# Optimization experiments

Measured on AMD Instinct MI355X. Metric: run time of the kernel, lower is better.

The kernel has to match this reference:

```python
import jax, jax.numpy as jnp
import numpy as np

B, L, D, H = 4, 2048, 1024, 16
d = D // H  # head_dim = 64
EPS = 1e-5
ROPE_BASE = 10000.0


def _rope_tables(seq_len, dim):
    inv_freq = 1.0 / (ROPE_BASE ** (jnp.arange(0, dim, 2, dtype=jnp.float32) / dim))
    t = jnp.arange(seq_len, dtype=jnp.float32)
    freqs = jnp.outer(t, inv_freq)                  # (L, d/2)
    emb = jnp.concatenate([freqs, freqs], axis=-1)  # (L, d)
    return jnp.cos(emb), jnp.sin(emb)


def _rotate_half(x):
    x1, x2 = jnp.split(x, 2, axis=-1)
    return jnp.concatenate([-x2, x1], axis=-1)


def setup_inputs() -> dict:
    key = jax.random.key(0)
    ks = jax.random.split(key, 5)
    x = jax.random.normal(ks[0], (B, L, D), dtype=jnp.float32)
    attn_mask = jnp.ones((B, 1, L, L), dtype=jnp.float32)
    conversion_mask = jax.random.uniform(ks[1], (B, L), dtype=jnp.float32)
    Wqkuv = jax.random.normal(ks[2], (D, 4 * D), dtype=jnp.float32) * (1.0 / np.sqrt(D))
    Wout = jax.random.normal(ks[3], (D, D), dtype=jnp.float32) * (1.0 / np.sqrt(D))
    ln_gamma = jnp.ones((d,), dtype=jnp.float32)
    ln_beta = jnp.zeros((d,), dtype=jnp.float32)
    conv_bias = jax.random.normal(ks[4], (H,), dtype=jnp.float32) * 0.02
    return {"x": x, "attn_mask": attn_mask, "conversion_mask": conversion_mask,
            "Wqkuv": Wqkuv, "Wout": Wout, "ln_gamma": ln_gamma,
            "ln_beta": ln_beta, "conv_bias": conv_bias}


def reference(x, attn_mask, conversion_mask, Wqkuv, Wout, ln_gamma, ln_beta, conv_bias):
    # qkuv projection with SiLU
    qkuv = jax.nn.silu(jnp.einsum('bld,de->ble', x, Wqkuv))  # (B, L, 4D)
    q, k, v, u = jnp.split(qkuv, 4, axis=-1)
    # reshape to (B, H, L, d)
    to_heads = lambda t: t.reshape(B, L, H, d).transpose(0, 2, 1, 3)
    q, k, v, u = map(to_heads, (q, k, v, u))
    # RoPE
    cos, sin = _rope_tables(L, d)            # (L, d)
    cos = cos[None, None]                    # (1,1,L,d)
    sin = sin[None, None]
    q = q * cos + _rotate_half(q) * sin
    k = k * cos + _rotate_half(k) * sin
    # scores + conversion bias + SiLU + multiplicative mask
    scores = jnp.einsum('bhld,bhmd->bhlm', q, k) / jnp.sqrt(jnp.float32(d))
    scores = scores + conversion_mask[:, None, None, :] * conv_bias[None, :, None, None]
    scores = jax.nn.silu(scores)
    scores = scores * attn_mask
    # attend, LayerNorm over head_dim, SiLU-gate with u
    attn_out = jnp.einsum('bhlm,bhmd->bhld', scores, v)
    mu = jnp.mean(attn_out, axis=-1, keepdims=True)
    var = jnp.var(attn_out, axis=-1, keepdims=True)
    attn_out = (attn_out - mu) / jnp.sqrt(var + EPS) * ln_gamma + ln_beta
    attn_out = attn_out * u
    attn_out = attn_out.transpose(0, 2, 1, 3).reshape(B, L, D)
    return jnp.einsum('bld,de->ble', attn_out, Wout)
```

## Files before the change

kernel.cpp:

```cpp
#include <hip/hip_runtime.h>
#include <math.h>

#define B_ 4
#define L_ 2048
#define D_ 1024
#define H_ 16

typedef __attribute__((ext_vector_type(4))) float f32x4;
typedef __attribute__((ext_vector_type(2))) float f32x2;
typedef __attribute__((ext_vector_type(8))) short s16x8;
typedef __attribute__((ext_vector_type(4))) short s16x4;
typedef __attribute__((ext_vector_type(4))) unsigned short u16x4;

__device__ __forceinline__ unsigned short f2bf(float f) {
  unsigned int u = __float_as_uint(f);
  u += 0x7fffu + ((u >> 16) & 1u);
  return (unsigned short)(u >> 16);
}
__device__ __forceinline__ float b2f(unsigned short s) {
  return __uint_as_float(((unsigned int)s) << 16);
}

__device__ __forceinline__ f32x4 mfma16x16x16_bf16(s16x4 a, s16x4 b, f32x4 c) {
#if __has_builtin(__builtin_amdgcn_mfma_f32_16x16x16bf16_1k)
  return __builtin_amdgcn_mfma_f32_16x16x16bf16_1k(a, b, c, 0, 0, 0);
#else
  f32x4 d;
  asm volatile("v_mfma_f32_16x16x16_bf16 %0, %1, %2, %3"
               : "=v"(d)
               : "v"(a), "v"(b), "v"(c));
  return d;
#endif
}

__global__ __launch_bounds__(256) void conv_x(const float* __restrict__ x,
                                              unsigned short* __restrict__ xb, int n4) {
  int i = blockIdx.x * 256 + threadIdx.x;
  if (i < n4) {
    f32x4 v = *(const f32x4*)(x + (size_t)i * 4);
    u16x4 o;
#pragma unroll
    for (int j = 0; j < 4; ++j) o[j] = f2bf(v[j]);
    *(u16x4*)(xb + (size_t)i * 4) = o;
  }
}

__global__ __launch_bounds__(256) void trans_w(const float* __restrict__ W,
                                               unsigned short* __restrict__ Wt,
                                               int K, int N) {
  __shared__ float T[64][65];
  const int k0 = blockIdx.y * 64, n0 = blockIdx.x * 64;
  const int tid = threadIdx.x;
#pragma unroll
  for (int i = 0; i < 16; ++i) {
    int e = tid + i * 256;
    int r = e >> 6, c = e & 63;
    T[r][c] = W[(size_t)(k0 + r) * N + n0 + c];
  }
  __syncthreads();
#pragma unroll
  for (int i = 0; i < 16; ++i) {
    int e = tid + i * 256;
    int r = e >> 6, c = e & 63;
    Wt[(size_t)(n0 + r) * K + k0 + c] = f2bf(T[c][r]);
  }
}

__global__ __launch_bounds__(256) void rope_tab(f32x2* __restrict__ tab) {
  int i = blockIdx.x * 256 + threadIdx.x;
  int l = i >> 5, j = i & 31;
  float inv = expf(-(float)j * (9.210340371976184f / 32.0f));
  float ang = (float)l * inv;
  f32x2 cs;
  cs[0] = cosf(ang);
  cs[1] = sinf(ang);
  tab[i] = cs;
}

template <int MODE>
__global__ __launch_bounds__(256) void gemm_bf16(const unsigned short* __restrict__ A,
                                                 const unsigned short* __restrict__ Bt,
                                                 void* __restrict__ Cp,
                                                 int M, int N, int K) {
  alignas(16) __shared__ unsigned short As[128][40];
  alignas(16) __shared__ unsigned short Bs[128][40];
  const int tid = threadIdx.x;
  const int lane = tid & 63, w = tid >> 6;
  const int quad = lane >> 4, l15 = lane & 15;
  const int wr = w >> 1, wc = w & 1;
  const int m0 = blockIdx.y * 128, n0 = blockIdx.x * 128;
  f32x4 acc[4][4] = {};
  for (int k0 = 0; k0 < K; k0 += 32) {
#pragma unroll
    for (int i = 0; i < 2; ++i) {
      int ch = tid + i * 256;
      int r = ch >> 2, c = ch & 3;
      *(s16x8*)&As[r][c * 8] = *(const s16x8*)(A + (size_t)(m0 + r) * K + k0 + c * 8);
      *(s16x8*)&Bs[r][c * 8] = *(const s16x8*)(Bt + (size_t)(n0 + r) * K + k0 + c * 8);
    }
    __syncthreads();
    s16x8 af[4], bf[4];
#pragma unroll
    for (int mi = 0; mi < 4; ++mi) af[mi] = *(const s16x8*)&As[wr * 64 + mi * 16 + l15][quad * 8];
#pragma unroll
    for (int nj = 0; nj < 4; ++nj) bf[nj] = *(const s16x8*)&Bs[wc * 64 + nj * 16 + l15][quad * 8];
#pragma unroll
    for (int mi = 0; mi < 4; ++mi)
#pragma unroll
      for (int nj = 0; nj < 4; ++nj)
        acc[mi][nj] = __builtin_amdgcn_mfma_f32_16x16x32_bf16(af[mi], bf[nj], acc[mi][nj], 0, 0, 0);
    __syncthreads();
  }
#pragma unroll
  for (int mi = 0; mi < 4; ++mi)
#pragma unroll
    for (int nj = 0; nj < 4; ++nj)
#pragma unroll
      for (int reg = 0; reg < 4; ++reg) {
        int rg = m0 + wr * 64 + mi * 16 + quad * 4 + reg;
        int cg = n0 + wc * 64 + nj * 16 + l15;
        float v = acc[mi][nj][reg];
        if (MODE == 1) {
          v = v / (1.0f + __expf(-v));
          ((unsigned short*)Cp)[(size_t)rg * N + cg] = f2bf(v);
        } else {
          ((float*)Cp)[(size_t)rg * N + cg] = v;
        }
      }
}

__global__ __launch_bounds__(256) void rope_conv(unsigned short* __restrict__ qk,
                                                 unsigned short* __restrict__ vt,
                                                 const f32x2* __restrict__ tab) {
  alignas(16) __shared__ unsigned short Vsh[64][72];
  const int tid = threadIdx.x;
  const int bh = blockIdx.y, b = bh >> 4, h = bh & 15;
  const int l0 = blockIdx.x * 64;
#pragma unroll
  for (int i = 0; i < 2; ++i) {
    int p = tid + i * 256;
    int row = p >> 3, c4 = p & 7;
    int l = l0 + row;
    size_t base = (size_t)(b * L_ + l) * 4096 + h * 64 + c4 * 4;
#pragma unroll
    for (int t = 0; t < 2; ++t) {
      size_t o = base + (size_t)t * 1024;
      u16x4 lo = *(u16x4*)(qk + o);
      u16x4 hi = *(u16x4*)(qk + o + 32);
      u16x4 nlo, nhi;
#pragma unroll
      for (int jj = 0; jj < 4; ++jj) {
        f32x2 cs = tab[l * 32 + c4 * 4 + jj];
        float fl = b2f(lo[jj]), fh = b2f(hi[jj]);
        nlo[jj] = f2bf(fl * cs[0] - fh * cs[1]);
        nhi[jj] = f2bf(fh * cs[0] + fl * cs[1]);
      }
      *(u16x4*)(qk + o) = nlo;
      *(u16x4*)(qk + o + 32) = nhi;
    }
  }
#pragma unroll
  for (int i = 0; i < 2; ++i) {
    int ch = tid + i * 256;
    int row = ch >> 3, c8 = ch & 7;
    *(s16x8*)&Vsh[row][c8 * 8] =
        *(const s16x8*)(qk + (size_t)(b * L_ + l0 + row) * 4096 + 2048 + h * 64 + c8 * 8);
  }
  __syncthreads();
#pragma unroll
  for (int i = 0; i < 2; ++i) {
    int ch = tid + i * 256;
    int drow = ch >> 3, c8 = ch & 7;
    s16x8 o;
#pragma unroll
    for (int jj = 0; jj < 8; ++jj) o[jj] = (short)Vsh[c8 * 8 + jj][drow];
    *(s16x8*)(vt + (size_t)(bh * 64 + drow) * 2048 + l0 + c8 * 8) = o;
  }
}

__global__ __launch_bounds__(256) void attn_mfma(
    const unsigned short* __restrict__ qk, const unsigned short* __restrict__ vt,
    const float* __restrict__ amask, const float* __restrict__ cmask,
    const float* __restrict__ cbias, const float* __restrict__ gamma,
    const float* __restrict__ beta, unsigned short* __restrict__ attng) {
  alignas(16) __shared__ unsigned short Ks[64][72];
  alignas(16) __shared__ unsigned short Vts[64][72];
  const int tid = threadIdx.x;
  const int lane = tid & 63, w = tid >> 6;
  const int quad = lane >> 4, l15 = lane & 15;
  const int bh = blockIdx.y, b = bh >> 4, h = bh & 15;
  const int l0 = blockIdx.x * 128;
  const float cb = cbias[h];

  s16x8 qf[2][2];
#pragma unroll
  for (int qs = 0; qs < 2; ++qs) {
    int qg = l0 + w * 32 + qs * 16 + l15;
#pragma unroll
    for (int s = 0; s < 2; ++s)
      qf[qs][s] = *(const s16x8*)(qk + (size_t)(b * L_ + qg) * 4096 + h * 64 + s * 32 + quad * 8);
  }

  f32x4 oacc[2][4] = {};

  for (int m0 = 0; m0 < L_; m0 += 64) {
    __syncthreads();
#pragma unroll
    for (int i = 0; i < 2; ++i) {
      int ch = tid + i * 256;
      int r = ch >> 3, c = ch & 7;
      *(s16x8*)&Ks[r][c * 8] =
          *(const s16x8*)(qk + (size_t)(b * L_ + m0 + r) * 4096 + 1024 + h * 64 + c * 8);
      *(s16x8*)&Vts[r][c * 8] = *(const s16x8*)(vt + (size_t)(bh * 64 + r) * 2048 + m0 + c * 8);
    }
    f32x4 cm4[4], am4[2][4];
#pragma unroll
    for (int kt = 0; kt < 4; ++kt)
      cm4[kt] = *(const f32x4*)(cmask + (size_t)b * L_ + m0 + kt * 16 + quad * 4);
#pragma unroll
    for (int qs = 0; qs < 2; ++qs) {
      int qg = l0 + w * 32 + qs * 16 + l15;
#pragma unroll
      for (int kt = 0; kt < 4; ++kt)
        am4[qs][kt] =
            *(const f32x4*)(amask + ((size_t)b * L_ + qg) * L_ + m0 + kt * 16 + quad * 4);
    }
    __syncthreads();

    f32x4 sacc[2][4] = {};
#pragma unroll
    for (int s = 0; s < 2; ++s) {
      s16x8 kf[4];
#pragma unroll
      for (int kt = 0; kt < 4; ++kt)
        kf[kt] = *(const s16x8*)&Ks[kt * 16 + l15][s * 32 + quad * 8];
#pragma unroll
      for (int qs = 0; qs < 2; ++qs)
#pragma unroll
        for (int kt = 0; kt < 4; ++kt)
          sacc[qs][kt] = __builtin_amdgcn_mfma_f32_16x16x32_bf16(kf[kt], qf[qs][s],
                                                                 sacc[qs][kt], 0, 0, 0);
    }

    s16x4 pf[2][4];
#pragma unroll
    for (int qs = 0; qs < 2; ++qs)
#pragma unroll
      for (int kt = 0; kt < 4; ++kt) {
#pragma unroll
        for (int r = 0; r < 4; ++r) {
          float v = sacc[qs][kt][r] * 0.125f + cm4[kt][r] * cb;
          v = v / (1.0f + __expf(-v));
          v *= am4[qs][kt][r];
          pf[qs][kt][r] = (short)f2bf(v);
        }
      }

#pragma unroll
    for (int dt = 0; dt < 4; ++dt)
#pragma unroll
      for (int kt = 0; kt < 4; ++kt) {
        s16x4 vf = *(const s16x4*)&Vts[dt * 16 + l15][kt * 16 + quad * 4];
#pragma unroll
        for (int qs = 0; qs < 2; ++qs)
          oacc[qs][dt] = mfma16x16x16_bf16(pf[qs][kt], vf, oacc[qs][dt]);
      }
  }

  const float ga = gamma[0 * 16 + l15];
#pragma unroll
  for (int qs = 0; qs < 2; ++qs) {
    float sm[4], sq[4];
#pragma unroll
    for (int reg = 0; reg < 4; ++reg) {
      float s1 = 0.f, s2 = 0.f;
#pragma unroll
      for (int dt = 0; dt < 4; ++dt) {
        float v = oacc[qs][dt][reg];
        s1 += v;
        s2 += v * v;
      }
      sm[reg] = s1;
      sq[reg] = s2;
    }
#pragma unroll
    for (int m = 1; m < 16; m <<= 1) {
#pragma unroll
      for (int reg = 0; reg < 4; ++reg) {
        sm[reg] += __shfl_xor(sm[reg], m);
        sq[reg] += __shfl_xor(sq[reg], m);
      }
    }
    float mu[4], rs[4];
#pragma unroll
    for (int reg = 0; reg < 4; ++reg) {
      mu[reg] = sm[reg] * (1.0f / 64.0f);
      float var = sq[reg] * (1.0f / 64.0f) - mu[reg] * mu[reg];
      rs[reg] = rsqrtf(var + 1e-5f);
    }
#pragma unroll
    for (int dt = 0; dt < 4; ++dt) {
      float g = gamma[dt * 16 + l15], be = beta[dt * 16 + l15];
#pragma unroll
      for (int reg = 0; reg < 4; ++reg) {
        int rowg = l0 + w * 32 + qs * 16 + quad * 4 + reg;
        int colg = dt * 16 + l15;
        float v = (oacc[qs][dt][reg] - mu[reg]) * rs[reg] * g + be;
        float u = b2f(qk[(size_t)(b * L_ + rowg) * 4096 + 3072 + h * 64 + colg]);
        attng[(size_t)(b * L_ + rowg) * 1024 + h * 64 + colg] = f2bf(v * u);
      }
    }
  }
  (void)ga;
}

extern "C" void kernel_launch(void* const* d_in, const int* in_sizes, int n_in,
                              void* d_out, int out_size, void* d_ws, size_t ws_size,
                              hipStream_t stream) {
  const float* x = (const float*)d_in[0];
  const float* amask = (const float*)d_in[1];
  const float* cmask = (const float*)d_in[2];
  const float* Wqkuv = (const float*)d_in[3];
  const float* Wout = (const float*)d_in[4];
  const float* gamma = (const float*)d_in[5];
  const float* beta = (const float*)d_in[6];
  const float* cbias = (const float*)d_in[7];
  float* out = (float*)d_out;

  char* ws = (char*)d_ws;
  unsigned short* qkuv_bf = (unsigned short*)ws;
  unsigned short* vt = (unsigned short*)(ws + ((size_t)64 << 20));
  unsigned short* xbf = (unsigned short*)(ws + ((size_t)80 << 20));
  unsigned short* Wt = (unsigned short*)(ws + ((size_t)96 << 20));
  unsigned short* Wot = (unsigned short*)(ws + ((size_t)104 << 20));
  unsigned short* attng = (unsigned short*)(ws + ((size_t)106 << 20));
  f32x2* tab = (f32x2*)(ws + ((size_t)122 << 20));

  conv_x<<<8192, 256, 0, stream>>>(x, xbf, (B_ * L_ * D_) / 4);
  trans_w<<<dim3(4096 / 64, 1024 / 64), 256, 0, stream>>>(Wqkuv, Wt, 1024, 4096);
  trans_w<<<dim3(1024 / 64, 1024 / 64), 256, 0, stream>>>(Wout, Wot, 1024, 1024);
  rope_tab<<<(L_ * 32) / 256, 256, 0, stream>>>(tab);

  gemm_bf16<1><<<dim3(4096 / 128, 8192 / 128), 256, 0, stream>>>(xbf, Wt, qkuv_bf,
                                                                 B_ * L_, 4 * D_, D_);
  rope_conv<<<dim3(L_ / 64, B_ * H_), 256, 0, stream>>>(qkuv_bf, vt, tab);
  attn_mfma<<<dim3(L_ / 128, B_ * H_), 256, 0, stream>>>(qkuv_bf, vt, amask, cmask, cbias,
                                                         gamma, beta, attng);
  gemm_bf16<0><<<dim3(1024 / 128, 8192 / 128), 256, 0, stream>>>(attng, Wot, out,
                                                                 B_ * L_, D_, D_);
}
```

Baseline: 529.5 us.

## Use direct global-to-LDS loads with XOR swizzle in GEMM, fast SiLU

```diff
diff --git a/kernel.cpp b/kernel.cpp
--- a/kernel.cpp
+++ b/kernel.cpp
@@ -1,5 +1,6 @@
 #include <hip/hip_runtime.h>
 #include <math.h>
+#include <stdint.h>
 
 #define B_ 4
 #define L_ 2048
@@ -19,6 +20,14 @@
 }
 __device__ __forceinline__ float b2f(unsigned short s) {
   return __uint_as_float(((unsigned int)s) << 16);
+}
+__device__ __forceinline__ float silu_fast(float v) {
+  return v * __builtin_amdgcn_rcpf(1.0f + __expf(-v));
+}
+__device__ __forceinline__ void gl_lds16(const void* g, void* l) {
+  __builtin_amdgcn_global_load_lds(
+      (__attribute__((address_space(1))) void*)(uintptr_t)g,
+      (__attribute__((address_space(3))) void*)(uint32_t)(uintptr_t)l, 16, 0, 0);
 }
 
 __device__ __forceinline__ f32x4 mfma16x16x16_bf16(s16x4 a, s16x4 b, f32x4 c) {
@@ -82,34 +91,36 @@
                                                  const unsigned short* __restrict__ Bt,
                                                  void* __restrict__ Cp,
                                                  int M, int N, int K) {
-  alignas(16) __shared__ unsigned short As[128][40];
-  alignas(16) __shared__ unsigned short Bs[128][40];
+  alignas(16) __shared__ unsigned short As[128][32];
+  alignas(16) __shared__ unsigned short Bs[128][32];
   const int tid = threadIdx.x;
   const int lane = tid & 63, w = tid >> 6;
   const int quad = lane >> 4, l15 = lane & 15;
   const int wr = w >> 1, wc = w & 1;
   const int m0 = blockIdx.y * 128, n0 = blockIdx.x * 128;
+  const int srow = lane >> 2;
+  const int schunk = (lane & 3) ^ ((lane >> 3) & 3);
+  const int fcol = (quad ^ ((l15 >> 1) & 3)) * 8;
   f32x4 acc[4][4] = {};
   for (int k0 = 0; k0 < K; k0 += 32) {
+    __syncthreads();
 #pragma unroll
     for (int i = 0; i < 2; ++i) {
-      int ch = tid + i * 256;
-      int r = ch >> 2, c = ch & 3;
-      *(s16x8*)&As[r][c * 8] = *(const s16x8*)(A + (size_t)(m0 + r) * K + k0 + c * 8);
-      *(s16x8*)&Bs[r][c * 8] = *(const s16x8*)(Bt + (size_t)(n0 + r) * K + k0 + c * 8);
+      int r0 = (w * 2 + i) * 16;
+      gl_lds16(A + (size_t)(m0 + r0 + srow) * K + k0 + schunk * 8, &As[r0][0]);
+      gl_lds16(Bt + (size_t)(n0 + r0 + srow) * K + k0 + schunk * 8, &Bs[r0][0]);
     }
     __syncthreads();
     s16x8 af[4], bf[4];
 #pragma unroll
-    for (int mi = 0; mi < 4; ++mi) af[mi] = *(const s16x8*)&As[wr * 64 + mi * 16 + l15][quad * 8];
-#pragma unroll
-    for (int nj = 0; nj < 4; ++nj) bf[nj] = *(const s16x8*)&Bs[wc * 64 + nj * 16 + l15][quad * 8];
+    for (int mi = 0; mi < 4; ++mi) af[mi] = *(const s16x8*)&As[wr * 64 + mi * 16 + l15][fcol];
+#pragma unroll
+    for (int nj = 0; nj < 4; ++nj) bf[nj] = *(const s16x8*)&Bs[wc * 64 + nj * 16 + l15][fcol];
 #pragma unroll
     for (int mi = 0; mi < 4; ++mi)
 #pragma unroll
       for (int nj = 0; nj < 4; ++nj)
         acc[mi][nj] = __builtin_amdgcn_mfma_f32_16x16x32_bf16(af[mi], bf[nj], acc[mi][nj], 0, 0, 0);
-    __syncthreads();
   }
 #pragma unroll
   for (int mi = 0; mi < 4; ++mi)
@@ -121,8 +132,7 @@
         int cg = n0 + wc * 64 + nj * 16 + l15;
         float v = acc[mi][nj][reg];
         if (MODE == 1) {
-          v = v / (1.0f + __expf(-v));
-          ((unsigned short*)Cp)[(size_t)rg * N + cg] = f2bf(v);
+          ((unsigned short*)Cp)[(size_t)rg * N + cg] = f2bf(silu_fast(v));
         } else {
           ((float*)Cp)[(size_t)rg * N + cg] = v;
         }
@@ -213,10 +223,12 @@
           *(const s16x8*)(qk + (size_t)(b * L_ + m0 + r) * 4096 + 1024 + h * 64 + c * 8);
       *(s16x8*)&Vts[r][c * 8] = *(const s16x8*)(vt + (size_t)(bh * 64 + r) * 2048 + m0 + c * 8);
     }
-    f32x4 cm4[4], am4[2][4];
-#pragma unroll
-    for (int kt = 0; kt < 4; ++kt)
-      cm4[kt] = *(const f32x4*)(cmask + (size_t)b * L_ + m0 + kt * 16 + quad * 4);
+    f32x4 cmcb[4], am4[2][4];
+#pragma unroll
+    for (int kt = 0; kt < 4; ++kt) {
+      f32x4 cm = *(const f32x4*)(cmask + (size_t)b * L_ + m0 + kt * 16 + quad * 4);
+      cmcb[kt] = cm * cb;
+    }
 #pragma unroll
     for (int qs = 0; qs < 2; ++qs) {
       int qg = l0 + w * 32 + qs * 16 + l15;
@@ -249,8 +261,8 @@
       for (int kt = 0; kt < 4; ++kt) {
 #pragma unroll
         for (int r = 0; r < 4; ++r) {
-          float v = sacc[qs][kt][r] * 0.125f + cm4[kt][r] * cb;
-          v = v / (1.0f + __expf(-v));
+          float v = fmaf(sacc[qs][kt][r], 0.125f, cmcb[kt][r]);
+          v = silu_fast(v);
           v *= am4[qs][kt][r];
           pf[qs][kt][r] = (short)f2bf(v);
         }
@@ -267,7 +279,6 @@
       }
   }
 
-  const float ga = gamma[0 * 16 + l15];
 #pragma unroll
   for (int qs = 0; qs < 2; ++qs) {
     float sm[4], sq[4];
@@ -311,7 +322,6 @@
       }
     }
   }
-  (void)ga;
 }
 
 extern "C" void kernel_launch(void* const* d_in, const int* in_sizes, int n_in,
```

After: 468.8 us. 11.5% less time.
